# Optimization experiments

Measured on AMD Instinct MI355X. Metric: run time of the kernel, lower is better.

The kernel has to match this reference:

```python
import jax, jax.numpy as jnp
import numpy as np

B, C, N = 8, 512, 2048
C2 = C // 2
BN_EPS = 1e-5


def setup_inputs() -> dict:
    key = jax.random.key(0)
    ks = jax.random.split(key, 8)
    s = lambda fan_in: 1.0 / np.sqrt(fan_in)
    return {
        "q": jax.random.normal(ks[0], (B, C, N), jnp.float32),
        "x": jax.random.normal(ks[1], (B, C2, N), jnp.float32),
        "Wq": jax.random.normal(ks[2], (C2, C), jnp.float32) * s(C),
        "Wk": jax.random.normal(ks[3], (C2, C2), jnp.float32) * s(C2),
        "Wv": jax.random.normal(ks[4], (C2, C), jnp.float32) * s(C),
        "bv": jax.random.normal(ks[5], (C2,), jnp.float32) * 0.01,
        "Wt": jax.random.normal(ks[6], (C2, C2), jnp.float32) * s(C2),
        "bt": jax.random.normal(ks[7], (C2,), jnp.float32) * 0.01,
        "gamma": jnp.ones((C2,), jnp.float32),
        "beta": jnp.zeros((C2,), jnp.float32),
        "running_mean": jnp.zeros((C2,), jnp.float32),
        "running_var": jnp.ones((C2,), jnp.float32),
    }


def reference(q, x, Wq, Wk, Wv, bv, Wt, bt, gamma, beta, running_mean, running_var):
    # 1x1 convs are pointwise GEMMs over the channel dim
    x_q = jnp.einsum("oc,bcn->bno", Wq, q)                    # [B, N, C2]
    x_k = jnp.einsum("oc,bcn->bon", Wk, x)                    # [B, C2, N]
    x_v = jnp.einsum("oc,bcn->bon", Wv, q) + bv[None, :, None]  # [B, C2, N]
    energy = jnp.einsum("bnc,bcm->bnm", x_q, x_k)             # [B, N, N]
    attn = jax.nn.softmax(energy, axis=-1)
    # offset-attention L1 renormalization over the query axis (dim=1)
    attn = attn / (1e-9 + attn.sum(axis=1, keepdims=True))
    x_r = jnp.einsum("bcn,bnm->bcm", x_v, attn)               # [B, C2, N]
    h = jnp.einsum("oc,bcn->bon", Wt, x - x_r) + bt[None, :, None]
    # BatchNorm1d in eval mode with running statistics
    inv = gamma / jnp.sqrt(running_var + BN_EPS)
    h = h * inv[None, :, None] + (beta - running_mean * inv)[None, :, None]
    return jax.nn.relu(h) + x
```

## Files before the change

### kernel.cpp

```cpp
#include <hip/hip_runtime.h>
#include <cstdint>
#include <cstddef>

#define KB_  8
#define KC_  512
#define KC2_ 256
#define KN_  2048

typedef __attribute__((ext_vector_type(8))) __bf16 bf16x8;
typedef __attribute__((ext_vector_type(8))) unsigned short u16x8;
typedef __attribute__((ext_vector_type(4))) float f32x4;

__device__ __forceinline__ unsigned short f2bf(float f) {
  union { float f; unsigned u; } x; x.f = f;
  unsigned r = x.u + 0x7fffu + ((x.u >> 16) & 1u);
  return (unsigned short)(r >> 16);
}
__device__ __forceinline__ float bf2f(unsigned short h) {
  union { unsigned u; float f; } x; x.u = ((unsigned)h) << 16;
  return x.f;
}

#define GLD16(g, l) __builtin_amdgcn_global_load_lds( \
    (__attribute__((address_space(1))) void*)(g),     \
    (__attribute__((address_space(3))) void*)(l), 16, 0, 0)

#define WAIT_VM8()  asm volatile("s_waitcnt vmcnt(8)" ::: "memory")
#define WAIT_VM0()  asm volatile("s_waitcnt vmcnt(0)" ::: "memory")
#define BARRIER()   __builtin_amdgcn_s_barrier()

__device__ __forceinline__ void xcd_swizzle(int& bx, int& by, int& bz) {
  const int gx = gridDim.x, gy = gridDim.y;
  const int nb = gx * gy * (int)gridDim.z;
  int f = ((int)blockIdx.z * gy + (int)blockIdx.y) * gx + (int)blockIdx.x;
  if ((nb & 7) == 0) f = (f & 7) * (nb >> 3) + (f >> 3);
  const int gxy = gx * gy;
  bz = f / gxy; int rem = f - bz * gxy;
  by = rem / gx; bx = rem - by * gx;
}

__global__ __launch_bounds__(256) void cvt_kernel(const float* __restrict__ in,
                                                  unsigned short* __restrict__ out, int n) {
  int i = (blockIdx.x * 256 + threadIdx.x) * 4;
  if (i >= n) return;
  float4 f = *(const float4*)(in + i);
  ushort4 u = { f2bf(f.x), f2bf(f.y), f2bf(f.z), f2bf(f.w) };
  *(ushort4*)(out + i) = u;
}

__global__ __launch_bounds__(256) void cvt_pair_kernel(const float* __restrict__ in,
                                                       unsigned short* __restrict__ hi,
                                                       unsigned short* __restrict__ lo, int n) {
  int i = (blockIdx.x * 256 + threadIdx.x) * 4;
  if (i >= n) return;
  float4 f = *(const float4*)(in + i);
  ushort4 h = { f2bf(f.x), f2bf(f.y), f2bf(f.z), f2bf(f.w) };
  ushort4 l = { f2bf(f.x - bf2f(h.x)), f2bf(f.y - bf2f(h.y)),
                f2bf(f.z - bf2f(h.z)), f2bf(f.w - bf2f(h.w)) };
  *(ushort4*)(hi + i) = h;
  *(ushort4*)(lo + i) = l;
}

__global__ __launch_bounds__(256) void transpose_pair_kernel(const float* __restrict__ in,
                                                             long sIn,
                                                             unsigned short* __restrict__ hi,
                                                             unsigned short* __restrict__ lo,
                                                             long sOut, int R, int Cc) {
  int b = blockIdx.z;
  const float* I = in + (size_t)b * sIn;
  __shared__ float tile[64][65];
  int t = threadIdx.x;
  int r0 = blockIdx.y * 64, c0 = blockIdx.x * 64;
#pragma unroll
  for (int k = 0; k < 4; k++) {
    int vi = k * 256 + t, rr = vi >> 4, cv = vi & 15;
    float4 f = *(const float4*)&I[(size_t)(r0 + rr) * Cc + c0 + cv * 4];
    tile[rr][cv * 4 + 0] = f.x; tile[rr][cv * 4 + 1] = f.y;
    tile[rr][cv * 4 + 2] = f.z; tile[rr][cv * 4 + 3] = f.w;
  }
  __syncthreads();
#pragma unroll
  for (int k = 0; k < 4; k++) {
    int vi = k * 256 + t, cc = vi >> 4, rv = vi & 15;
    float f0 = tile[rv * 4 + 0][cc], f1 = tile[rv * 4 + 1][cc];
    float f2 = tile[rv * 4 + 2][cc], f3 = tile[rv * 4 + 3][cc];
    ushort4 h = { f2bf(f0), f2bf(f1), f2bf(f2), f2bf(f3) };
    ushort4 l = { f2bf(f0 - bf2f(h.x)), f2bf(f1 - bf2f(h.y)),
                  f2bf(f2 - bf2f(h.z)), f2bf(f3 - bf2f(h.w)) };
    size_t o = (size_t)b * sOut + (size_t)(c0 + cc) * R + r0 + rv * 4;
    *(ushort4*)&hi[o] = h;
    *(ushort4*)&lo[o] = l;
  }
}

__global__ __launch_bounds__(256) void rowreduce_kernel(const float* __restrict__ rowpart,
                                                        float* __restrict__ rsv) {
  int idx = blockIdx.x * 256 + threadIdx.x;
  const float* p = rowpart + (size_t)idx * 32;
  float s = 0.f;
#pragma unroll
  for (int k = 0; k < 32; k++) s += p[k];
  rsv[idx] = 1.0f / s;
}

__global__ __launch_bounds__(256) void denom_kernel(const unsigned short* __restrict__ uT,
                                                    const float* __restrict__ rsv,
                                                    float* __restrict__ denom) {
  int b = blockIdx.y;
  int m = blockIdx.x * 4 + (threadIdx.x >> 6);
  int lane = threadIdx.x & 63;
  const unsigned short* U = uT + ((size_t)b * KN_ + m) * KN_;
  const float* R = rsv + (size_t)b * KN_;
  float s = 0.f;
#pragma unroll
  for (int c = 0; c < 4; c++) {
    int n = c * 512 + lane * 8;
    u16x8 u = *(const u16x8*)&U[n];
    float4 r0 = *(const float4*)&R[n];
    float4 r1 = *(const float4*)&R[n + 4];
    s += bf2f(u[0]) * r0.x + bf2f(u[1]) * r0.y + bf2f(u[2]) * r0.z + bf2f(u[3]) * r0.w;
    s += bf2f(u[4]) * r1.x + bf2f(u[5]) * r1.y + bf2f(u[6]) * r1.z + bf2f(u[7]) * r1.w;
  }
#pragma unroll
  for (int o = 32; o > 0; o >>= 1) s += __shfl_xor(s, o, 64);
  if (lane == 0) denom[(size_t)b * KN_ + m] = s;
}

__global__ __launch_bounds__(256) void energy_kernel(
    const unsigned short* __restrict__ Ahi, const unsigned short* __restrict__ Alo,
    const unsigned short* __restrict__ Bhi, const unsigned short* __restrict__ Blo,
    unsigned short* __restrict__ uT, float* __restrict__ rowpart) {
  int bx, by, b;
  xcd_swizzle(bx, by, b);
  Ahi += (size_t)b * KN_ * KC2_; Alo += (size_t)b * KN_ * KC2_;
  Bhi += (size_t)b * KN_ * KC2_; Blo += (size_t)b * KN_ * KC2_;
  const int m0 = by * 128;
  const int n0 = bx * 128;
  __shared__ __align__(16) char smem[65536];
  const int t = threadIdx.x, lane = t & 63, w = t >> 6;
  const int wr = w >> 1, wc = w & 1;
  const int srow = t >> 2;
  const int scol = (((t & 3) ^ ((srow >> 1) & 3)) * 8);
  const int lr = lane & 15, lk = (lane >> 4) * 8;
  const int rsw = ((lr >> 1) & 3) << 4;

  auto STAGE = [&](char* dst, int kt) {
    const size_t ga = (size_t)(m0 + srow) * KC2_ + kt + scol;
    const size_t gb = (size_t)(n0 + srow) * KC2_ + kt + scol;
    GLD16(Ahi + ga, dst + 0 + w * 1024);
    GLD16(Ahi + ga + (size_t)64 * KC2_, dst + 4096 + w * 1024);
    GLD16(Alo + ga, dst + 8192 + w * 1024);
    GLD16(Alo + ga + (size_t)64 * KC2_, dst + 12288 + w * 1024);
    GLD16(Bhi + gb, dst + 16384 + w * 1024);
    GLD16(Bhi + gb + (size_t)64 * KC2_, dst + 20480 + w * 1024);
    GLD16(Blo + gb, dst + 24576 + w * 1024);
    GLD16(Blo + gb + (size_t)64 * KC2_, dst + 28672 + w * 1024);
  };

  f32x4 acc[4][4];
  const f32x4 z = {0.f, 0.f, 0.f, 0.f};
#pragma unroll
  for (int i = 0; i < 4; i++)
#pragma unroll
    for (int j = 0; j < 4; j++) acc[i][j] = z;

  STAGE(smem, 0);
  for (int kt8 = 0; kt8 < 8; kt8++) {
    char* cur = smem + (kt8 & 1) * 32768;
    char* nxt = smem + ((kt8 & 1) ^ 1) * 32768;
    if (kt8 < 7) {
      STAGE(nxt, (kt8 + 1) * 32);
      WAIT_VM8();
    } else {
      WAIT_VM0();
    }
    BARRIER();
    bf16x8 ah[4], al[4], bh[4], bl[4];
#pragma unroll
    for (int i = 0; i < 4; i++) {
      int ro = (wr * 64 + i * 16 + lr) * 64 + ((lk * 2) ^ rsw);
      ah[i] = *(const bf16x8*)(cur + 0 + ro);
      al[i] = *(const bf16x8*)(cur + 8192 + ro);
    }
#pragma unroll
    for (int j = 0; j < 4; j++) {
      int ro = (wc * 64 + j * 16 + lr) * 64 + ((lk * 2) ^ rsw);
      bh[j] = *(const bf16x8*)(cur + 16384 + ro);
      bl[j] = *(const bf16x8*)(cur + 24576 + ro);
    }
#pragma unroll
    for (int i = 0; i < 4; i++)
#pragma unroll
      for (int j = 0; j < 4; j++) {
        acc[i][j] = __builtin_amdgcn_mfma_f32_16x16x32_bf16(al[i], bh[j], acc[i][j], 0, 0, 0);
        acc[i][j] = __builtin_amdgcn_mfma_f32_16x16x32_bf16(ah[i], bl[j], acc[i][j], 0, 0, 0);
        acc[i][j] = __builtin_amdgcn_mfma_f32_16x16x32_bf16(ah[i], bh[j], acc[i][j], 0, 0, 0);
      }
    BARRIER();
  }

#pragma unroll
  for (int i = 0; i < 4; i++)
#pragma unroll
    for (int j = 0; j < 4; j++)
#pragma unroll
      for (int r = 0; r < 4; r++) acc[i][j][r] = __expf(acc[i][j][r] - 40.f);

#pragma unroll
  for (int i = 0; i < 4; i++) {
#pragma unroll
    for (int r = 0; r < 4; r++) {
      float s = acc[i][0][r] + acc[i][1][r] + acc[i][2][r] + acc[i][3][r];
      s += __shfl_xor(s, 1, 64); s += __shfl_xor(s, 2, 64);
      s += __shfl_xor(s, 4, 64); s += __shfl_xor(s, 8, 64);
      if ((lane & 15) == 0) {
        int row = m0 + wr * 64 + i * 16 + ((lane >> 4) << 2) + r;
        rowpart[((size_t)b * KN_ + row) * 32 + bx * 2 + wc] = s;
      }
    }
  }

#pragma unroll
  for (int i = 0; i < 4; i++) {
#pragma unroll
    for (int j = 0; j < 4; j++) {
#pragma unroll
      for (int r2 = 0; r2 < 4; r2 += 2) {
        int qn = wr * 64 + i * 16 + ((lane >> 4) << 2) + r2;
        int km = wc * 64 + j * 16 + lr;
        unsigned pk = (unsigned)f2bf(acc[i][j][r2]) |
                      ((unsigned)f2bf(acc[i][j][r2 + 1]) << 16);
        int a = ((km << 8) + (qn << 1)) ^ ((km & 15) << 4);
        *(unsigned*)(smem + a) = pk;
      }
    }
  }
  __syncthreads();
#pragma unroll
  for (int it = 0; it < 8; it++) {
    int km = (t >> 4) + it * 16, chunk = t & 15;
    int a = ((km << 8) + (chunk << 4)) ^ ((km & 15) << 4);
    size_t g = ((size_t)b * KN_ + (n0 + km)) * KN_ + m0 + chunk * 8;
    *(bf16x8*)&uT[g] = *(const bf16x8*)(smem + a);
  }
}

enum { EPI_PAIR = 0, EPI_VSCALE = 2, EPI_PART = 3, EPI_FINAL = 4 };

struct EpiParams {
  const float* bias;
  const float* xf;  long xf_stride;
  const float* scale; long scale_stride;
  const float* gamma; const float* beta; const float* mean; const float* var;
};

template<int EPI>
__device__ __forceinline__ void gemm_core(
    char* __restrict__ smem, int bx, int by, int b,
    const unsigned short* __restrict__ A0, const unsigned short* __restrict__ A1,
    long sA, int lda, int seg,
    const unsigned short* __restrict__ B0, const unsigned short* __restrict__ B1,
    long sB, int ldb,
    void* __restrict__ Cv, void* __restrict__ Cv2, long sC, int ldc, int K,
    const EpiParams& ep) {
  A0 += (size_t)b * sA; A1 += (size_t)b * sA;
  B0 += (size_t)b * sB; B1 += (size_t)b * sB;
  const int m0 = by * 128, n0 = bx * 128;
  const int t = threadIdx.x, lane = t & 63, w = t >> 6;
  const int wr = w >> 1, wc = w & 1;
  const int srow = t >> 2;
  const int scol = (((t & 3) ^ ((srow >> 1) & 3)) * 8);
  const int lr = lane & 15, lk = (lane >> 4) * 8;
  const int rsw = ((lr >> 1) & 3) << 4;

  auto STAGE = [&](char* dst, int kt) {
    int s = seg ? ((kt >= seg) + (kt >= 2 * seg)) : 0;
    int kl = kt - s * seg;
    const unsigned short* Ab = (s == 1) ? A1 : A0;
    const unsigned short* Bb = (s == 2) ? B1 : B0;
    const unsigned short* gA = Ab + (size_t)(m0 + srow) * lda + kl + scol;
    const unsigned short* gB = Bb + (size_t)(n0 + srow) * ldb + kl + scol;
    GLD16(gA, dst + w * 1024);
    GLD16(gA + (size_t)64 * lda, dst + 4096 + w * 1024);
    GLD16(gA + 32, dst + 8192 + w * 1024);
    GLD16(gA + (size_t)64 * lda + 32, dst + 12288 + w * 1024);
    GLD16(gB, dst + 16384 + w * 1024);
    GLD16(gB + (size_t)64 * ldb, dst + 20480 + w * 1024);
    GLD16(gB + 32, dst + 24576 + w * 1024);
    GLD16(gB + (size_t)64 * ldb + 32, dst + 28672 + w * 1024);
  };

  f32x4 acc[4][4];
  const f32x4 z = {0.f, 0.f, 0.f, 0.f};
#pragma unroll
  for (int i = 0; i < 4; i++)
#pragma unroll
    for (int j = 0; j < 4; j++) acc[i][j] = z;

  const int nt = K >> 6;
  STAGE(smem, 0);
  for (int t8 = 0; t8 < nt; t8++) {
    char* cur = smem + (t8 & 1) * 32768;
    char* nxt = smem + ((t8 & 1) ^ 1) * 32768;
    if (t8 < nt - 1) {
      STAGE(nxt, (t8 + 1) * 64);
      WAIT_VM8();
    } else {
      WAIT_VM0();
    }
    BARRIER();
#pragma unroll
    for (int kk = 0; kk < 2; kk++) {
      bf16x8 af[4], bfv[4];
#pragma unroll
      for (int i = 0; i < 4; i++)
        af[i] = *(const bf16x8*)(cur + kk * 8192 +
                                 (wr * 64 + i * 16 + lr) * 64 + ((lk * 2) ^ rsw));
#pragma unroll
      for (int j = 0; j < 4; j++)
        bfv[j] = *(const bf16x8*)(cur + 16384 + kk * 8192 +
                                  (wc * 64 + j * 16 + lr) * 64 + ((lk * 2) ^ rsw));
#pragma unroll
      for (int i = 0; i < 4; i++)
#pragma unroll
        for (int j = 0; j < 4; j++)
          acc[i][j] = __builtin_amdgcn_mfma_f32_16x16x32_bf16(af[i], bfv[j], acc[i][j], 0, 0, 0);
    }
    BARRIER();
  }

#pragma unroll
  for (int i = 0; i < 4; i++) {
#pragma unroll
    for (int r = 0; r < 4; r++) {
      const int row = m0 + wr * 64 + i * 16 + ((lane >> 4) << 2) + r;
      float pbias = 0.f, pinv = 1.f, padd = 0.f;
      if constexpr (EPI == EPI_VSCALE) pbias = ep.bias[row];
      if constexpr (EPI == EPI_FINAL) {
        pbias = ep.bias[row];
        float iv = ep.gamma[row] * rsqrtf(ep.var[row] + 1e-5f);
        pinv = iv;
        padd = ep.beta[row] - ep.mean[row] * iv;
      }
#pragma unroll
      for (int j = 0; j < 4; j++) {
        const int col = n0 + wc * 64 + j * 16 + lr;
        float v = acc[i][j][r];
        size_t o = (size_t)b * sC + (size_t)row * ldc + col;
        if constexpr (EPI == EPI_PAIR) {
          unsigned short h = f2bf(v);
          ((unsigned short*)Cv)[o] = h;
          ((unsigned short*)Cv2)[o] = f2bf(v - bf2f(h));
        } else if constexpr (EPI == EPI_VSCALE) {
          float sc = ep.scale[(size_t)b * ep.scale_stride + col];
          ((unsigned short*)Cv)[o] = f2bf((v + pbias) * sc);
        } else if constexpr (EPI == EPI_PART) {
          ((float*)Cv)[o] = v;
        } else {
          float h = (v + pbias) * pinv + padd;
          h = fmaxf(h, 0.f);
          float xval = ep.xf[(size_t)b * ep.xf_stride + o - (size_t)b * sC];
          ((float*)Cv)[o] = h + xval;
        }
      }
    }
  }
}

template<int EPI>
__global__ __launch_bounds__(256) void gemm_one(
    const unsigned short* __restrict__ A0, const unsigned short* __restrict__ A1,
    long sA, int lda, int seg,
    const unsigned short* __restrict__ B0, const unsigned short* __restrict__ B1,
    long sB, int ldb,
    void* __restrict__ Cv, void* __restrict__ Cv2, long sC, int ldc, int K,
    EpiParams ep) {
  __shared__ __align__(16) char smem[65536];
  int bx, by, b;
  xcd_swizzle(bx, by, b);
  gemm_core<EPI>(smem, bx, by, b, A0, A1, sA, lda, seg, B0, B1, sB, ldb,
                 Cv, Cv2, sC, ldc, K, ep);
}

__global__ __launch_bounds__(256) void proj2_kernel(
    const unsigned short* __restrict__ qThi, const unsigned short* __restrict__ qTlo,
    const unsigned short* __restrict__ Wqhi, const unsigned short* __restrict__ Wqlo,
    unsigned short* __restrict__ xqhi, unsigned short* __restrict__ xqlo,
    const unsigned short* __restrict__ xThi, const unsigned short* __restrict__ xTlo,
    const unsigned short* __restrict__ Wkhi, const unsigned short* __restrict__ Wklo,
    unsigned short* __restrict__ xkhi, unsigned short* __restrict__ xklo) {
  __shared__ __align__(16) char smem[65536];
  int f = (int)blockIdx.x;
  f = (f & 7) * 64 + (f >> 3);
  EpiParams ep{};
  if (f < 256) {
    int bx = f & 1, by = (f >> 1) & 15, b = f >> 5;
    gemm_core<EPI_PAIR>(smem, bx, by, b, qThi, qTlo, (long)KN_ * KC_, KC_, KC_,
                        Wqhi, Wqlo, 0, KC_, xqhi, xqlo, (long)KN_ * KC2_, KC2_,
                        3 * KC_, ep);
  } else {
    int g = f - 256;
    int bx = g & 1, by = (g >> 1) & 15, b = g >> 5;
    gemm_core<EPI_PAIR>(smem, bx, by, b, xThi, xTlo, (long)KN_ * KC2_, KC2_, KC2_,
                        Wkhi, Wklo, 0, KC2_, xkhi, xklo, (long)KN_ * KC2_, KC2_,
                        3 * KC2_, ep);
  }
}

__global__ __launch_bounds__(256) void xr_kernel(
    const unsigned short* __restrict__ x_v, const unsigned short* __restrict__ uT,
    float* __restrict__ P) {
  __shared__ __align__(16) char smem[65536];
  int bx, by, b;
  xcd_swizzle(bx, by, b);
  int split = bx >> 4; bx &= 15;
  EpiParams ep{};
  gemm_core<EPI_PART>(smem, bx, by, b,
                      x_v + split * (KN_ / 2), nullptr, (long)KC2_ * KN_, KN_, 0,
                      uT + split * (KN_ / 2), nullptr, (long)KN_ * KN_, KN_,
                      P + (size_t)split * KB_ * KC2_ * KN_, nullptr,
                      (long)KC2_ * KN_, KN_, KN_ / 2, ep);
}

__global__ __launch_bounds__(256) void xr_reduce_kernel(
    const float* __restrict__ P, const float* __restrict__ x,
    const float* __restrict__ denom, unsigned short* __restrict__ tT) {
  int b = blockIdx.z;
  const float* P0 = P + (size_t)b * KC2_ * KN_;
  const float* P1 = P0 + (size_t)KB_ * KC2_ * KN_;
  const float* X  = x + (size_t)b * KC2_ * KN_;
  const float* D  = denom + (size_t)b * KN_;
  __shared__ unsigned short tile[64][72];
  int t = threadIdx.x;
  int c0 = blockIdx.y * 64, m0 = blockIdx.x * 64;
#pragma unroll
  for (int k = 0; k < 4; k++) {
    int vi = k * 256 + t, rr = vi >> 4, cv = vi & 15;
    size_t o = (size_t)(c0 + rr) * KN_ + m0 + cv * 4;
    float4 p0 = *(const float4*)&P0[o];
    float4 p1 = *(const float4*)&P1[o];
    float4 xv = *(const float4*)&X[o];
    float4 dv = *(const float4*)&D[m0 + cv * 4];
    tile[rr][cv * 4 + 0] = f2bf(xv.x - (p0.x + p1.x) / (1e-9f + dv.x));
    tile[rr][cv * 4 + 1] = f2bf(xv.y - (p0.y + p1.y) / (1e-9f + dv.y));
    tile[rr][cv * 4 + 2] = f2bf(xv.z - (p0.z + p1.z) / (1e-9f + dv.z));
    tile[rr][cv * 4 + 3] = f2bf(xv.w - (p0.w + p1.w) / (1e-9f + dv.w));
  }
  __syncthreads();
#pragma unroll
  for (int k = 0; k < 4; k++) {
    int vi = k * 256 + t, cc = vi >> 4, rv = vi & 15;
    ushort4 u = { tile[rv * 4 + 0][cc], tile[rv * 4 + 1][cc],
                  tile[rv * 4 + 2][cc], tile[rv * 4 + 3][cc] };
    *(ushort4*)&tT[(size_t)b * KN_ * KC2_ + (size_t)(m0 + cc) * KC2_ + c0 + rv * 4] = u;
  }
}

extern "C" void kernel_launch(void* const* d_in, const int* in_sizes, int n_in,
                              void* d_out, int out_size, void* d_ws, size_t ws_size,
                              hipStream_t stream) {
  (void)in_sizes; (void)n_in; (void)out_size; (void)ws_size;
  const float* q     = (const float*)d_in[0];
  const float* x     = (const float*)d_in[1];
  const float* Wq    = (const float*)d_in[2];
  const float* Wk    = (const float*)d_in[3];
  const float* Wv    = (const float*)d_in[4];
  const float* bv    = (const float*)d_in[5];
  const float* Wt    = (const float*)d_in[6];
  const float* bt    = (const float*)d_in[7];
  const float* gamma = (const float*)d_in[8];
  const float* beta  = (const float*)d_in[9];
  const float* rmean = (const float*)d_in[10];
  const float* rvar  = (const float*)d_in[11];
  float* out = (float*)d_out;

  const size_t SZ_qT = (size_t)KB_ * KN_ * KC_ * 2;
  const size_t SZ_xT = (size_t)KB_ * KN_ * KC2_ * 2;
  char* ws = (char*)d_ws;
  size_t off = 0;
  auto alloc = [&](size_t bytes) {
    char* p = ws + off;
    off += (bytes + 255) & ~(size_t)255;
    return p;
  };
  unsigned short* qThi = (unsigned short*)alloc(SZ_qT);
  unsigned short* qTlo = (unsigned short*)alloc(SZ_qT);
  unsigned short* xThi = (unsigned short*)alloc(SZ_xT);
  unsigned short* xTlo = (unsigned short*)alloc(SZ_xT);
  unsigned short* xqhi = (unsigned short*)alloc(SZ_xT);
  unsigned short* xqlo = (unsigned short*)alloc(SZ_xT);
  unsigned short* xkhi = (unsigned short*)alloc(SZ_xT);
  unsigned short* xklo = (unsigned short*)alloc(SZ_xT);
  unsigned short* x_v  = (unsigned short*)alloc((size_t)KB_ * KC2_ * KN_ * 2);
  unsigned short* tT   = (unsigned short*)alloc(SZ_xT);
  unsigned short* Wqhi = (unsigned short*)alloc((size_t)KC2_ * KC_ * 2);
  unsigned short* Wqlo = (unsigned short*)alloc((size_t)KC2_ * KC_ * 2);
  unsigned short* Wkhi = (unsigned short*)alloc((size_t)KC2_ * KC2_ * 2);
  unsigned short* Wklo = (unsigned short*)alloc((size_t)KC2_ * KC2_ * 2);
  unsigned short* Wvb  = (unsigned short*)alloc((size_t)KC2_ * KC_ * 2);
  unsigned short* Wtb  = (unsigned short*)alloc((size_t)KC2_ * KC2_ * 2);
  float* rsv     = (float*)alloc((size_t)KB_ * KN_ * 4);
  float* denom   = (float*)alloc((size_t)KB_ * KN_ * 4);
  float* rowpart = (float*)alloc((size_t)KB_ * KN_ * 32 * 4);
  float* P       = (float*)alloc((size_t)2 * KB_ * KC2_ * KN_ * 4);
  unsigned short* uT = (unsigned short*)alloc((size_t)KB_ * KN_ * KN_ * 2);

  dim3 blk(256);

  cvt_pair_kernel<<<dim3(KC2_ * KC_ / 1024), blk, 0, stream>>>(Wq, Wqhi, Wqlo, KC2_ * KC_);
  cvt_pair_kernel<<<dim3(KC2_ * KC2_ / 1024), blk, 0, stream>>>(Wk, Wkhi, Wklo, KC2_ * KC2_);
  cvt_kernel<<<dim3(KC2_ * KC_ / 1024), blk, 0, stream>>>(Wv, Wvb, KC2_ * KC_);
  cvt_kernel<<<dim3(KC2_ * KC2_ / 1024), blk, 0, stream>>>(Wt, Wtb, KC2_ * KC2_);

  transpose_pair_kernel<<<dim3(KN_ / 64, KC_ / 64, KB_), blk, 0, stream>>>(
      q, (long)KC_ * KN_, qThi, qTlo, (long)KN_ * KC_, KC_, KN_);
  transpose_pair_kernel<<<dim3(KN_ / 64, KC2_ / 64, KB_), blk, 0, stream>>>(
      x, (long)KC2_ * KN_, xThi, xTlo, (long)KN_ * KC2_, KC2_, KN_);

  proj2_kernel<<<dim3(512), blk, 0, stream>>>(qThi, qTlo, Wqhi, Wqlo, xqhi, xqlo,
                                              xThi, xTlo, Wkhi, Wklo, xkhi, xklo);

  energy_kernel<<<dim3(KN_ / 128, KN_ / 128, KB_), blk, 0, stream>>>(
      xqhi, xqlo, xkhi, xklo, uT, rowpart);
  rowreduce_kernel<<<dim3(KB_ * KN_ / 256), blk, 0, stream>>>(rowpart, rsv);

  EpiParams e3{}; e3.bias = bv; e3.scale = rsv; e3.scale_stride = KN_;
  gemm_one<EPI_VSCALE><<<dim3(KN_ / 128, KC2_ / 128, KB_), blk, 0, stream>>>(
      Wvb, nullptr, 0, KC_, 0, qThi, nullptr, (long)KN_ * KC_, KC_,
      x_v, nullptr, (long)KC2_ * KN_, KN_, KC_, e3);

  denom_kernel<<<dim3(KN_ / 4, KB_), blk, 0, stream>>>(uT, rsv, denom);

  xr_kernel<<<dim3(32, 2, 8), blk, 0, stream>>>(x_v, uT, P);
  xr_reduce_kernel<<<dim3(KN_ / 64, KC2_ / 64, KB_), blk, 0, stream>>>(P, x, denom, tT);

  EpiParams e6{}; e6.bias = bt; e6.xf = x; e6.xf_stride = (long)KC2_ * KN_;
  e6.gamma = gamma; e6.beta = beta; e6.mean = rmean; e6.var = rvar;
  gemm_one<EPI_FINAL><<<dim3(KN_ / 128, KC2_ / 128, KB_), blk, 0, stream>>>(
      Wtb, nullptr, 0, KC2_, 0, tT, nullptr, (long)KN_ * KC2_, KC2_,
      out, nullptr, (long)KC2_ * KN_, KN_, KC2_, e6);
}
```

Measured before the change: 207.2 us.

## Fuse xr GEMM with residual, denominator scaling and transpose epilogue, drop split-K

```diff
diff --git a/kernel.cpp b/kernel.cpp
--- a/kernel.cpp
+++ b/kernel.cpp
@@ -245,7 +245,7 @@
   }
 }
 
-enum { EPI_PAIR = 0, EPI_VSCALE = 2, EPI_PART = 3, EPI_FINAL = 4 };
+enum { EPI_PAIR = 0, EPI_VSCALE = 2, EPI_XRT = 3, EPI_FINAL = 4 };
 
 struct EpiParams {
   const float* bias;
@@ -329,6 +329,43 @@
     BARRIER();
   }
 
+  if constexpr (EPI == EPI_XRT) {
+    float dinv[4];
+#pragma unroll
+    for (int j = 0; j < 4; j++)
+      dinv[j] = 1.0f / (1e-9f + ep.scale[(size_t)b * ep.scale_stride +
+                                         n0 + wc * 64 + j * 16 + lr]);
+    const float* X = ep.xf + (size_t)b * ep.xf_stride;
+#pragma unroll
+    for (int i = 0; i < 4; i++) {
+#pragma unroll
+      for (int j = 0; j < 4; j++) {
+#pragma unroll
+        for (int r2 = 0; r2 < 4; r2 += 2) {
+          int cl = wr * 64 + i * 16 + ((lane >> 4) << 2) + r2;
+          int ml = wc * 64 + j * 16 + lr;
+          float x0 = X[(size_t)(m0 + cl) * KN_ + n0 + ml];
+          float x1 = X[(size_t)(m0 + cl + 1) * KN_ + n0 + ml];
+          float t0 = x0 - acc[i][j][r2] * dinv[j];
+          float t1 = x1 - acc[i][j][r2 + 1] * dinv[j];
+          unsigned pk = (unsigned)f2bf(t0) | ((unsigned)f2bf(t1) << 16);
+          int a = ((ml << 8) + (cl << 1)) ^ ((ml & 15) << 4);
+          *(unsigned*)(smem + a) = pk;
+        }
+      }
+    }
+    __syncthreads();
+    unsigned short* tT = (unsigned short*)Cv;
+#pragma unroll
+    for (int it = 0; it < 8; it++) {
+      int ml = (t >> 4) + it * 16, chunk = t & 15;
+      int a = ((ml << 8) + (chunk << 4)) ^ ((ml & 15) << 4);
+      size_t g = ((size_t)b * KN_ + (n0 + ml)) * KC2_ + m0 + chunk * 8;
+      *(bf16x8*)&tT[g] = *(const bf16x8*)(smem + a);
+    }
+    return;
+  }
+
 #pragma unroll
   for (int i = 0; i < 4; i++) {
 #pragma unroll
@@ -354,8 +391,6 @@
         } else if constexpr (EPI == EPI_VSCALE) {
           float sc = ep.scale[(size_t)b * ep.scale_stride + col];
           ((unsigned short*)Cv)[o] = f2bf((v + pbias) * sc);
-        } else if constexpr (EPI == EPI_PART) {
-          ((float*)Cv)[o] = v;
         } else {
           float h = (v + pbias) * pinv + padd;
           h = fmaxf(h, 0.f);
@@ -404,55 +439,6 @@
     gemm_core<EPI_PAIR>(smem, bx, by, b, xThi, xTlo, (long)KN_ * KC2_, KC2_, KC2_,
                         Wkhi, Wklo, 0, KC2_, xkhi, xklo, (long)KN_ * KC2_, KC2_,
                         3 * KC2_, ep);
-  }
-}
-
-__global__ __launch_bounds__(256) void xr_kernel(
-    const unsigned short* __restrict__ x_v, const unsigned short* __restrict__ uT,
-    float* __restrict__ P) {
-  __shared__ __align__(16) char smem[65536];
-  int bx, by, b;
-  xcd_swizzle(bx, by, b);
-  int split = bx >> 4; bx &= 15;
-  EpiParams ep{};
-  gemm_core<EPI_PART>(smem, bx, by, b,
-                      x_v + split * (KN_ / 2), nullptr, (long)KC2_ * KN_, KN_, 0,
-                      uT + split * (KN_ / 2), nullptr, (long)KN_ * KN_, KN_,
-                      P + (size_t)split * KB_ * KC2_ * KN_, nullptr,
-                      (long)KC2_ * KN_, KN_, KN_ / 2, ep);
-}
-
-__global__ __launch_bounds__(256) void xr_reduce_kernel(
-    const float* __restrict__ P, const float* __restrict__ x,
-    const float* __restrict__ denom, unsigned short* __restrict__ tT) {
-  int b = blockIdx.z;
-  const float* P0 = P + (size_t)b * KC2_ * KN_;
-  const float* P1 = P0 + (size_t)KB_ * KC2_ * KN_;
-  const float* X  = x + (size_t)b * KC2_ * KN_;
-  const float* D  = denom + (size_t)b * KN_;
-  __shared__ unsigned short tile[64][72];
-  int t = threadIdx.x;
-  int c0 = blockIdx.y * 64, m0 = blockIdx.x * 64;
-#pragma unroll
-  for (int k = 0; k < 4; k++) {
-    int vi = k * 256 + t, rr = vi >> 4, cv = vi & 15;
-    size_t o = (size_t)(c0 + rr) * KN_ + m0 + cv * 4;
-    float4 p0 = *(const float4*)&P0[o];
-    float4 p1 = *(const float4*)&P1[o];
-    float4 xv = *(const float4*)&X[o];
-    float4 dv = *(const float4*)&D[m0 + cv * 4];
-    tile[rr][cv * 4 + 0] = f2bf(xv.x - (p0.x + p1.x) / (1e-9f + dv.x));
-    tile[rr][cv * 4 + 1] = f2bf(xv.y - (p0.y + p1.y) / (1e-9f + dv.y));
-    tile[rr][cv * 4 + 2] = f2bf(xv.z - (p0.z + p1.z) / (1e-9f + dv.z));
-    tile[rr][cv * 4 + 3] = f2bf(xv.w - (p0.w + p1.w) / (1e-9f + dv.w));
-  }
-  __syncthreads();
-#pragma unroll
-  for (int k = 0; k < 4; k++) {
-    int vi = k * 256 + t, cc = vi >> 4, rv = vi & 15;
-    ushort4 u = { tile[rv * 4 + 0][cc], tile[rv * 4 + 1][cc],
-                  tile[rv * 4 + 2][cc], tile[rv * 4 + 3][cc] };
-    *(ushort4*)&tT[(size_t)b * KN_ * KC2_ + (size_t)(m0 + cc) * KC2_ + c0 + rv * 4] = u;
   }
 }
 
@@ -502,7 +488,6 @@
   float* rsv     = (float*)alloc((size_t)KB_ * KN_ * 4);
   float* denom   = (float*)alloc((size_t)KB_ * KN_ * 4);
   float* rowpart = (float*)alloc((size_t)KB_ * KN_ * 32 * 4);
-  float* P       = (float*)alloc((size_t)2 * KB_ * KC2_ * KN_ * 4);
   unsigned short* uT = (unsigned short*)alloc((size_t)KB_ * KN_ * KN_ * 2);
 
   dim3 blk(256);
@@ -531,8 +516,11 @@
 
   denom_kernel<<<dim3(KN_ / 4, KB_), blk, 0, stream>>>(uT, rsv, denom);
 
-  xr_kernel<<<dim3(32, 2, 8), blk, 0, stream>>>(x_v, uT, P);
-  xr_reduce_kernel<<<dim3(KN_ / 64, KC2_ / 64, KB_), blk, 0, stream>>>(P, x, denom, tT);
+  EpiParams e5{}; e5.xf = x; e5.xf_stride = (long)KC2_ * KN_;
+  e5.scale = denom; e5.scale_stride = KN_;
+  gemm_one<EPI_XRT><<<dim3(KN_ / 128, KC2_ / 128, KB_), blk, 0, stream>>>(
+      x_v, nullptr, (long)KC2_ * KN_, KN_, 0, uT, nullptr, (long)KN_ * KN_, KN_,
+      tT, nullptr, 0, 0, KN_, e5);
 
   EpiParams e6{}; e6.bias = bt; e6.xf = x; e6.xf_stride = (long)KC2_ * KN_;
   e6.gamma = gamma; e6.beta = beta; e6.mean = rmean; e6.var = rvar;
```

Result: faster. 197.2 us (-4.8%).
